# Kernel tuning notes

Measured on AMD Instinct MI355X. Metric: run time of the kernel, lower is better.

## Reference

```python
import jax, jax.numpy as jnp
import numpy as np

DEFAULT_MASK_VALUE = -0.7 * float(jnp.finfo(jnp.dtype('float32')).max)

B, T, NQ, NKV, D = 2, 1024, 32, 8, 128


def setup_inputs() -> dict:
    key = jax.random.key(0)
    k1, k2, k3, k4 = jax.random.split(key, 4)
    query = jax.random.normal(k1, (B, T, NQ, D), dtype=jnp.float32)
    kk = jax.random.normal(k2, (B, T, NKV, D), dtype=jnp.float32)
    vv = jax.random.normal(k3, (B, T, NKV, D), dtype=jnp.float32)
    # packed-sequence segment ids, sorted so each segment is contiguous (values 1..3, >0 = active)
    decoder_segment_ids = jnp.sort(jax.random.randint(k4, (B, T), 1, 4), axis=-1).astype(jnp.int32)
    return {"query": query, "key": kk, "value": vv,
            "decoder_segment_ids": decoder_segment_ids}


def _attention(query, key, value, decoder_segment_ids):
    # MaxText AttentionOp.apply_attention_dot (prefill / train mode), GQA layout.
    b, t, n, d = query.shape
    n_kv = key.shape[2]
    g = n // n_kv
    q = query.reshape(b, t, n_kv, g, d)
    # qk product: [b, n_kv, g, t, s]
    logits = jnp.einsum('btkgd,bskd->bkgts', q, key)
    # generate_attention_mask: segment mask AND causal mask
    seg_mask = decoder_segment_ids[:, :, None] == decoder_segment_ids[:, None, :]  # [b,t,s]
    row_ids = jax.lax.broadcasted_iota(jnp.int32, (t, t), 0)
    col_ids = jax.lax.broadcasted_iota(jnp.int32, (t, t), 1)
    causal = col_ids <= row_ids  # [t,s]
    mask = jnp.logical_and(seg_mask, causal[None])  # [b,t,s]
    # apply_mask_to_logits: replace masked entries with DEFAULT_MASK_VALUE (avoids add fusion)
    masked = jnp.where(mask[:, None, None, :, :], logits, DEFAULT_MASK_VALUE)
    probs = jax.nn.softmax(masked, axis=-1)
    out = jnp.einsum('bkgts,bskd->btkgd', probs, value)
    return out.reshape(b, t, n, d)


def reference(query, key, value, decoder_segment_ids):
    return _attention(query, key, value, decoder_segment_ids)
```

## Files before the change

### kernel.cpp

```cpp
#include <hip/hip_runtime.h>

constexpr int B_  = 2;
constexpr int T_  = 1024;
constexpr int NQ  = 32;
constexpr int NKV = 8;
constexpr int D_  = 128;

constexpr int BM = 64;
constexpr int BN = 64;
constexpr int NTILE = T_ / BM;
constexpr float MASK_NEG = -3.0e38f;

typedef _Float16 f16;
typedef f16 f16x4 __attribute__((ext_vector_type(4)));
typedef f16 f16x8 __attribute__((ext_vector_type(8)));
typedef float floatx4 __attribute__((ext_vector_type(4)));

__device__ __align__(16) f16 g_K16 [(size_t)B_ * NKV * T_ * D_];
__device__ __align__(16) f16 g_Vt16[(size_t)B_ * NKV * T_ * D_];

__device__ __forceinline__ void dma16(const f16* g, const f16* l) {
    __builtin_amdgcn_global_load_lds(
        (const __attribute__((address_space(1))) void*)g,
        (__attribute__((address_space(3))) void*)l, 16, 0, 0);
}

__global__ __launch_bounds__(256)
void prep_kernel(const float* __restrict__ K, const float* __restrict__ V) {
    __shared__ f16 lv[64][136];
    const int sblk = blockIdx.x;
    const int kv   = blockIdx.y;
    const int b    = blockIdx.z;
    const int tid  = threadIdx.x;
    const int s0   = sblk * 64;
    const size_t inbase = ((size_t)b * T_) * NKV * D_ + (size_t)kv * D_;

    f16* kout = g_K16 + ((size_t)(b * NKV + kv) * T_ + s0) * D_;
#pragma unroll
    for (int p = 0; p < 4; ++p) {
        const int u = tid + 256 * p;
        const int s = u >> 4, ch = u & 15;
        const float* src = K + inbase + (size_t)(s0 + s) * NKV * D_ + ch * 8;
        float4 f0 = *(const float4*)src;
        float4 f1 = *(const float4*)(src + 4);
        f16x8 hh;
        hh[0] = (f16)f0.x; hh[1] = (f16)f0.y; hh[2] = (f16)f0.z; hh[3] = (f16)f0.w;
        hh[4] = (f16)f1.x; hh[5] = (f16)f1.y; hh[6] = (f16)f1.z; hh[7] = (f16)f1.w;
        *(f16x8*)(kout + s * D_ + ((ch ^ (s & 7)) * 8)) = hh;
    }
#pragma unroll
    for (int p = 0; p < 8; ++p) {
        const int u = tid + 256 * p;
        const int s = u >> 5, d4 = u & 31;
        float4 f = *(const float4*)(V + inbase + (size_t)(s0 + s) * NKV * D_ + d4 * 4);
        f16x4 hh; hh[0] = (f16)f.x; hh[1] = (f16)f.y; hh[2] = (f16)f.z; hh[3] = (f16)f.w;
        *(f16x4*)&lv[s][d4 * 4] = hh;
    }
    __syncthreads();
    f16* vout = g_Vt16 + (size_t)((b * NKV + kv) * 16 + sblk) * 8192;
#pragma unroll
    for (int p = 0; p < 4; ++p) {
        const int u = tid + 256 * p;
        const int d = u >> 3, cu = u & 7;
        f16x8 hh;
#pragma unroll
        for (int j = 0; j < 8; ++j) hh[j] = lv[cu * 8 + j][d];
        *(f16x8*)(vout + d * 64 + ((cu ^ (d & 7)) * 8)) = hh;
    }
}

#define FA_BODY(RK, RV, WK, WV, blkv)                                          \
    {                                                                          \
        const int s0 = (blkv) * BN;                                            \
        __syncthreads();                                                       \
        if ((blkv) + 1 < nblk) {                                               \
            const f16* kt = kbase + (size_t)((blkv) + 1) * 8192 + glane;       \
            const f16* vt = vbase + (size_t)((blkv) + 1) * 8192 + glane;       \
            _Pragma("unroll")                                                  \
            for (int i = 0; i < 4; ++i) {                                      \
                dma16(kt + i * 512, WK + wbase + i * 512);                     \
                dma16(vt + i * 512, WV + wbase + i * 512);                     \
            }                                                                  \
        }                                                                      \
        floatx4 sc[4];                                                         \
        _Pragma("unroll")                                                      \
        for (int nt = 0; nt < 4; ++nt) {                                       \
            floatx4 acc = floatx4{0.f, 0.f, 0.f, 0.f};                         \
            _Pragma("unroll")                                                  \
            for (int c = 0; c < 4; ++c) {                                      \
                f16x8 kf = *(const f16x8*)(RK + (nt * 16 + ln) * 128 + kpc[c]);\
                acc = __builtin_amdgcn_mfma_f32_16x16x32_f16(qfrag[c], kf, acc, 0, 0, 0); \
            }                                                                  \
            sc[nt] = acc;                                                      \
        }                                                                      \
        _Pragma("unroll")                                                      \
        for (int nt = 0; nt < 4; ++nt) {                                       \
            const int s = s0 + nt * 16 + ln;                                   \
            const int sgs = lds_seg[s];                                        \
            _Pragma("unroll")                                                  \
            for (int r = 0; r < 4; ++r) {                                      \
                const bool ok = (s <= trow[r]) && (sgs == segq[r]);            \
                sc[nt][r] = ok ? sc[nt][r] : MASK_NEG;                         \
            }                                                                  \
        }                                                                      \
        floatx4 av;                                                            \
        _Pragma("unroll")                                                      \
        for (int r = 0; r < 4; ++r) {                                          \
            float mx = fmaxf(fmaxf(sc[0][r], sc[1][r]), fmaxf(sc[2][r], sc[3][r])); \
            mx = fmaxf(mx, __shfl_xor(mx, 1));                                 \
            mx = fmaxf(mx, __shfl_xor(mx, 2));                                 \
            mx = fmaxf(mx, __shfl_xor(mx, 4));                                 \
            mx = fmaxf(mx, __shfl_xor(mx, 8));                                 \
            const float mnew = fmaxf(m_i[r], mx);                              \
            av[r] = __expf(m_i[r] - mnew);                                     \
            m_i[r] = mnew;                                                     \
            sc[0][r] = __expf(sc[0][r] - mnew);                                \
            sc[1][r] = __expf(sc[1][r] - mnew);                                \
            sc[2][r] = __expf(sc[2][r] - mnew);                                \
            sc[3][r] = __expf(sc[3][r] - mnew);                                \
        }                                                                      \
        _Pragma("unroll")                                                      \
        for (int dt = 0; dt < 9; ++dt) o_acc[dt] *= av;                        \
        _Pragma("unroll")                                                      \
        for (int nt = 0; nt < 4; ++nt)                                         \
            _Pragma("unroll")                                                  \
            for (int r = 0; r < 4; ++r)                                        \
                lds_p[wave][quad * 4 + r][nt * 16 + ln] = (f16)sc[nt][r];      \
        __builtin_amdgcn_s_waitcnt(0xc07f);               \
        f16x8 af0 = *(const f16x8*)&lds_p[wave][ln][quad * 8];                 \
        f16x8 af1 = *(const f16x8*)&lds_p[wave][ln][32 + quad * 8];            \
        _Pragma("unroll")                                                      \
        for (int dt = 0; dt < 8; ++dt) {                                       \
            const f16* vr = RV + (dt * 16 + ln) * 64;                          \
            f16x8 b0 = *(const f16x8*)(vr + pc0);                              \
            f16x8 b1 = *(const f16x8*)(vr + pc1);                              \
            o_acc[dt] = __builtin_amdgcn_mfma_f32_16x16x32_f16(af0, b0, o_acc[dt], 0, 0, 0); \
            o_acc[dt] = __builtin_amdgcn_mfma_f32_16x16x32_f16(af1, b1, o_acc[dt], 0, 0, 0); \
        }                                                                      \
        o_acc[8] = __builtin_amdgcn_mfma_f32_16x16x32_f16(af0, vones, o_acc[8], 0, 0, 0); \
        o_acc[8] = __builtin_amdgcn_mfma_f32_16x16x32_f16(af1, vones, o_acc[8], 0, 0, 0); \
    }

__global__ __launch_bounds__(256, 2)
void fa_kernel(const float* __restrict__ Qg, const int* __restrict__ seg,
               float* __restrict__ Og) {
    __shared__ __align__(16) f16 kb0[64 * 128];
    __shared__ __align__(16) f16 kb1[64 * 128];
    __shared__ __align__(16) f16 vb0[128 * 64];
    __shared__ __align__(16) f16 vb1[128 * 64];
    __shared__ f16 lds_p[4][16][72];
    __shared__ int lds_seg[T_];

    const int pair = blockIdx.x;
    const int h    = blockIdx.y;
    const int b    = blockIdx.z;
    const int kv   = h >> 2;

    const int tid  = threadIdx.x;
    const int wave = tid >> 6;
    const int lane = tid & 63;
    const int quad = lane >> 4;
    const int ln   = lane & 15;
    const int sw   = ln & 7;

    int kpc[4];
#pragma unroll
    for (int c = 0; c < 4; ++c) kpc[c] = ((4 * c + quad) ^ sw) * 8;
    const int pc0 = (quad ^ sw) * 8;
    const int pc1 = ((quad + 4) ^ sw) * 8;

    const int glane = wave * 2048 + lane * 8;
    const int wbase = wave * 2048;

    const f16* kbase = g_K16 + (size_t)(b * NKV + kv) * T_ * D_;
    const f16* vbase = g_Vt16 + (size_t)(b * NKV + kv) * T_ * D_;

    *(int4*)&lds_seg[tid * 4] = *(const int4*)(seg + b * T_ + tid * 4);

    f16x8 vones;
#pragma unroll
    for (int j = 0; j < 8; ++j) vones[j] = (f16)1.0f;

    for (int sub = 0; sub < 2; ++sub) {
        const int tile = sub ? pair : (NTILE - 1 - pair);
        const int t0 = tile * BM;

        const int qrow = t0 + wave * 16 + ln;
        const float* qptr = Qg + (((size_t)b * T_ + qrow) * NQ + h) * D_;
        f16x8 qfrag[4];
#pragma unroll
        for (int c = 0; c < 4; ++c) {
            const float* p = qptr + c * 32 + quad * 8;
            float4 f0 = *(const float4*)(p);
            float4 f1 = *(const float4*)(p + 4);
            f16x8 v;
            v[0] = (f16)f0.x; v[1] = (f16)f0.y; v[2] = (f16)f0.z; v[3] = (f16)f0.w;
            v[4] = (f16)f1.x; v[5] = (f16)f1.y; v[6] = (f16)f1.z; v[7] = (f16)f1.w;
            qfrag[c] = v;
        }

        __syncthreads();

        int trow[4], segq[4];
#pragma unroll
        for (int r = 0; r < 4; ++r) {
            trow[r] = t0 + wave * 16 + quad * 4 + r;
            segq[r] = lds_seg[trow[r]];
        }
        const int seg_lo = lds_seg[t0];

        unsigned long long bal = __ballot(lds_seg[lane * 16 + 15] < seg_lo);
        const int blk_start = __popcll(bal) >> 2;
        const int nblk = tile + 1;

        float  m_i[4];
        floatx4 o_acc[9];
#pragma unroll
        for (int r = 0; r < 4; ++r) m_i[r] = -1.0e30f;
#pragma unroll
        for (int dt = 0; dt < 9; ++dt) o_acc[dt] = floatx4{0.f, 0.f, 0.f, 0.f};

        {
            const f16* kt = kbase + (size_t)blk_start * 8192 + glane;
            const f16* vt = vbase + (size_t)blk_start * 8192 + glane;
#pragma unroll
            for (int i = 0; i < 4; ++i) {
                dma16(kt + i * 512, kb0 + wbase + i * 512);
                dma16(vt + i * 512, vb0 + wbase + i * 512);
            }
        }

        int blk = blk_start;
        while (true) {
            FA_BODY(kb0, vb0, kb1, vb1, blk)
            if (++blk >= nblk) break;
            FA_BODY(kb1, vb1, kb0, vb0, blk)
            if (++blk >= nblk) break;
        }

#pragma unroll
        for (int r = 0; r < 4; ++r) {
            const float inv = 1.0f / o_acc[8][r];
            float* optr = Og + (((size_t)b * T_ + trow[r]) * NQ + h) * D_ + ln;
#pragma unroll
            for (int dt = 0; dt < 8; ++dt)
                optr[dt * 16] = o_acc[dt][r] * inv;
        }
    }
}

extern "C" void kernel_launch(void* const* d_in, const int* in_sizes, int n_in,
                              void* d_out, int out_size, void* d_ws, size_t ws_size,
                              hipStream_t stream) {
    const float* Q   = (const float*)d_in[0];
    const float* K   = (const float*)d_in[1];
    const float* V   = (const float*)d_in[2];
    const int*   seg = (const int*)d_in[3];
    float* out = (float*)d_out;

    dim3 pgrid(NTILE, NKV, B_);
    prep_kernel<<<pgrid, 256, 0, stream>>>(K, V);

    dim3 grid(NTILE / 2, NQ, B_);
    fa_kernel<<<grid, 256, 0, stream>>>(Q, seg, out);
}
```

Measured before the change: 127.2 us.

## Compute transposed QK scores and shuffle P into MFMA fragments in registers

Swaps the MFMA operands so each lane holds scores for a single query row, which reduces the row max to two cross-lane shuffles and gives one running max per lane. The P matrix is packed to fp16 pairs and rearranged across lanes with xor shuffles instead of a round trip through an LDS staging buffer. The per-column segment compare is replaced by a range check against each row's segment start, found by binary search over the segment ids, which relies on segments being contiguous. The rescale factors are moved back to the output layout with ds_bpermute, which adds shuffle traffic in place of LDS stores and loads.

Result: faster. 124.6 us (-2.0%).

```diff
diff --git a/kernel.cpp b/kernel.cpp
--- a/kernel.cpp
+++ b/kernel.cpp
@@ -12,9 +12,11 @@
 constexpr float MASK_NEG = -3.0e38f;
 
 typedef _Float16 f16;
+typedef __fp16 fp16_2 __attribute__((ext_vector_type(2)));
 typedef f16 f16x4 __attribute__((ext_vector_type(4)));
 typedef f16 f16x8 __attribute__((ext_vector_type(8)));
 typedef float floatx4 __attribute__((ext_vector_type(4)));
+typedef unsigned int uintx4 __attribute__((ext_vector_type(4)));
 
 __device__ __align__(16) f16 g_K16 [(size_t)B_ * NKV * T_ * D_];
 __device__ __align__(16) f16 g_Vt16[(size_t)B_ * NKV * T_ * D_];
@@ -23,6 +25,30 @@
     __builtin_amdgcn_global_load_lds(
         (const __attribute__((address_space(1))) void*)g,
         (__attribute__((address_space(3))) void*)l, 16, 0, 0);
+}
+
+__device__ __forceinline__ void swap32(unsigned &a, unsigned &b) {
+    unsigned ax = (unsigned)__shfl_xor((int)a, 32);
+    unsigned bx = (unsigned)__shfl_xor((int)b, 32);
+    const bool hi = (threadIdx.x & 32) != 0;
+    unsigned na = hi ? bx : a;
+    unsigned nb = hi ? b  : ax;
+    a = na; b = nb;
+}
+
+__device__ __forceinline__ void swap16(unsigned &a, unsigned &b) {
+    unsigned ax = (unsigned)__shfl_xor((int)a, 16);
+    unsigned bx = (unsigned)__shfl_xor((int)b, 16);
+    const bool odd = (threadIdx.x & 16) != 0;
+    unsigned na = odd ? bx : a;
+    unsigned nb = odd ? b  : ax;
+    a = na; b = nb;
+}
+
+__device__ __forceinline__ unsigned pk2(float a, float b) {
+    union { fp16_2 h; unsigned u; } c;
+    c.h = __builtin_amdgcn_cvt_pkrtz(a, b);
+    return c.u;
 }
 
 __global__ __launch_bounds__(256)
@@ -89,46 +115,58 @@
             _Pragma("unroll")                                                  \
             for (int c = 0; c < 4; ++c) {                                      \
                 f16x8 kf = *(const f16x8*)(RK + (nt * 16 + ln) * 128 + kpc[c]);\
-                acc = __builtin_amdgcn_mfma_f32_16x16x32_f16(qfrag[c], kf, acc, 0, 0, 0); \
+                acc = __builtin_amdgcn_mfma_f32_16x16x32_f16(kf, qfrag[c], acc, 0, 0, 0); \
             }                                                                  \
             sc[nt] = acc;                                                      \
         }                                                                      \
         _Pragma("unroll")                                                      \
         for (int nt = 0; nt < 4; ++nt) {                                       \
-            const int s = s0 + nt * 16 + ln;                                   \
-            const int sgs = lds_seg[s];                                        \
             _Pragma("unroll")                                                  \
             for (int r = 0; r < 4; ++r) {                                      \
-                const bool ok = (s <= trow[r]) && (sgs == segq[r]);            \
+                const int s = s0 + nt * 16 + quad * 4 + r;                     \
+                const bool ok = (s <= qrow_l) && (s >= fs_l);                  \
                 sc[nt][r] = ok ? sc[nt][r] : MASK_NEG;                         \
             }                                                                  \
         }                                                                      \
-        floatx4 av;                                                            \
-        _Pragma("unroll")                                                      \
-        for (int r = 0; r < 4; ++r) {                                          \
-            float mx = fmaxf(fmaxf(sc[0][r], sc[1][r]), fmaxf(sc[2][r], sc[3][r])); \
-            mx = fmaxf(mx, __shfl_xor(mx, 1));                                 \
-            mx = fmaxf(mx, __shfl_xor(mx, 2));                                 \
-            mx = fmaxf(mx, __shfl_xor(mx, 4));                                 \
-            mx = fmaxf(mx, __shfl_xor(mx, 8));                                 \
-            const float mnew = fmaxf(m_i[r], mx);                              \
-            av[r] = __expf(m_i[r] - mnew);                                     \
-            m_i[r] = mnew;                                                     \
-            sc[0][r] = __expf(sc[0][r] - mnew);                                \
-            sc[1][r] = __expf(sc[1][r] - mnew);                                \
-            sc[2][r] = __expf(sc[2][r] - mnew);                                \
-            sc[3][r] = __expf(sc[3][r] - mnew);                                \
-        }                                                                      \
-        _Pragma("unroll")                                                      \
-        for (int dt = 0; dt < 9; ++dt) o_acc[dt] *= av;                        \
-        _Pragma("unroll")                                                      \
-        for (int nt = 0; nt < 4; ++nt)                                         \
-            _Pragma("unroll")                                                  \
-            for (int r = 0; r < 4; ++r)                                        \
-                lds_p[wave][quad * 4 + r][nt * 16 + ln] = (f16)sc[nt][r];      \
-        __builtin_amdgcn_s_waitcnt(0xc07f);               \
-        f16x8 af0 = *(const f16x8*)&lds_p[wave][ln][quad * 8];                 \
-        f16x8 af1 = *(const f16x8*)&lds_p[wave][ln][32 + quad * 8];            \
+        float mx = fmaxf(                                                      \
+            fmaxf(fmaxf(fmaxf(sc[0][0], sc[0][1]), fmaxf(sc[0][2], sc[0][3])), \
+                  fmaxf(fmaxf(sc[1][0], sc[1][1]), fmaxf(sc[1][2], sc[1][3]))),\
+            fmaxf(fmaxf(fmaxf(sc[2][0], sc[2][1]), fmaxf(sc[2][2], sc[2][3])), \
+                  fmaxf(fmaxf(sc[3][0], sc[3][1]), fmaxf(sc[3][2], sc[3][3]))));\
+        mx = fmaxf(mx, __shfl_xor(mx, 16));                                    \
+        mx = fmaxf(mx, __shfl_xor(mx, 32));                                    \
+        const float mnew = fmaxf(m_i, mx);                                     \
+        const float av = __expf(m_i - mnew);                                   \
+        m_i = mnew;                                                            \
+        _Pragma("unroll")                                                      \
+        for (int nt = 0; nt < 4; ++nt) {                                       \
+            sc[nt][0] = __expf(sc[nt][0] - mnew);                              \
+            sc[nt][1] = __expf(sc[nt][1] - mnew);                              \
+            sc[nt][2] = __expf(sc[nt][2] - mnew);                              \
+            sc[nt][3] = __expf(sc[nt][3] - mnew);                              \
+        }                                                                      \
+        const int avi = __float_as_int(av);                                    \
+        floatx4 avr;                                                           \
+        _Pragma("unroll")                                                      \
+        for (int r = 0; r < 4; ++r)                                            \
+            avr[r] = __int_as_float(__builtin_amdgcn_ds_bpermute(bpbase + 4 * r, avi)); \
+        _Pragma("unroll")                                                      \
+        for (int dt = 0; dt < 9; ++dt) o_acc[dt] *= avr;                       \
+        unsigned Da[4], Db[4];                                                 \
+        _Pragma("unroll")                                                      \
+        for (int nt = 0; nt < 4; ++nt) {                                       \
+            Da[nt] = pk2(sc[nt][0], sc[nt][1]);                                \
+            Db[nt] = pk2(sc[nt][2], sc[nt][3]);                                \
+        }                                                                      \
+        swap32(Da[0], Da[1]); swap32(Db[0], Db[1]);                            \
+        swap16(Da[0], Da[1]); swap16(Db[0], Db[1]);                            \
+        swap32(Da[2], Da[3]); swap32(Db[2], Db[3]);                            \
+        swap16(Da[2], Da[3]); swap16(Db[2], Db[3]);                            \
+        union { uintx4 u; f16x8 h; } c0_, c1_;                                 \
+        c0_.u = uintx4{Da[0], Db[0], Da[1], Db[1]};                            \
+        c1_.u = uintx4{Da[2], Db[2], Da[3], Db[3]};                            \
+        const f16x8 af0 = c0_.h;                                               \
+        const f16x8 af1 = c1_.h;                                               \
         _Pragma("unroll")                                                      \
         for (int dt = 0; dt < 8; ++dt) {                                       \
             const f16* vr = RV + (dt * 16 + ln) * 64;                          \
@@ -148,7 +186,6 @@
     __shared__ __align__(16) f16 kb1[64 * 128];
     __shared__ __align__(16) f16 vb0[128 * 64];
     __shared__ __align__(16) f16 vb1[128 * 64];
-    __shared__ f16 lds_p[4][16][72];
     __shared__ int lds_seg[T_];
 
     const int pair = blockIdx.x;
@@ -168,6 +205,7 @@
     for (int c = 0; c < 4; ++c) kpc[c] = ((4 * c + quad) ^ sw) * 8;
     const int pc0 = (quad ^ sw) * 8;
     const int pc1 = ((quad + 4) ^ sw) * 8;
+    const int bpbase = quad << 4;
 
     const int glane = wave * 2048 + lane * 8;
     const int wbase = wave * 2048;
@@ -201,22 +239,26 @@
 
         __syncthreads();
 
-        int trow[4], segq[4];
-#pragma unroll
-        for (int r = 0; r < 4; ++r) {
-            trow[r] = t0 + wave * 16 + quad * 4 + r;
-            segq[r] = lds_seg[trow[r]];
-        }
+        int trow[4];
+#pragma unroll
+        for (int r = 0; r < 4; ++r) trow[r] = t0 + wave * 16 + quad * 4 + r;
+
+        const int qrow_l = qrow;
+        const int segq_l = lds_seg[qrow_l];
+        int lo = 0, hi = qrow_l;
+        while (lo < hi) {
+            const int mid = (lo + hi) >> 1;
+            if (lds_seg[mid] < segq_l) lo = mid + 1; else hi = mid;
+        }
+        const int fs_l = lo;
+
         const int seg_lo = lds_seg[t0];
-
         unsigned long long bal = __ballot(lds_seg[lane * 16 + 15] < seg_lo);
         const int blk_start = __popcll(bal) >> 2;
         const int nblk = tile + 1;
 
-        float  m_i[4];
+        float  m_i = -1.0e30f;
         floatx4 o_acc[9];
-#pragma unroll
-        for (int r = 0; r < 4; ++r) m_i[r] = -1.0e30f;
 #pragma unroll
         for (int dt = 0; dt < 9; ++dt) o_acc[dt] = floatx4{0.f, 0.f, 0.f, 0.f};
 
```

## Use 128-row Q tiles with transposed S^T MFMA keeping P in registers

Applied to the files above, without the earlier changes.

Doubles the query tile to 128 rows, with each wave handling two 16-row groups that share the K/V fragments loaded from LDS. QK^T is computed transposed (K as the A operand) so the softmax probabilities land in the register layout the PV MFMA (16x16x16) expects. This removes the LDS round-trip for P and the ones-column MFMA used to get the row sum, which is now tracked as a scalar l_i. The segment mask becomes a per-row first-segment-start bound found by binary search, and blocks are ordered with a diagonal tile assignment instead of pairing heavy and light tiles. The cost is more registers per wave and possible load imbalance across tiles of different causal length.

After: 121.1 us. 4.8% less time.

```diff
diff --git a/kernel.cpp b/kernel.cpp
--- a/kernel.cpp
+++ b/kernel.cpp
@@ -6,12 +6,13 @@
 constexpr int NKV = 8;
 constexpr int D_  = 128;
 
-constexpr int BM = 64;
+constexpr int BM = 128;
 constexpr int BN = 64;
 constexpr int NTILE = T_ / BM;
 constexpr float MASK_NEG = -3.0e38f;
 
 typedef _Float16 f16;
+typedef __fp16 fp16_2 __attribute__((ext_vector_type(2)));
 typedef f16 f16x4 __attribute__((ext_vector_type(4)));
 typedef f16 f16x8 __attribute__((ext_vector_type(8)));
 typedef float floatx4 __attribute__((ext_vector_type(4)));
@@ -23,6 +24,12 @@
     __builtin_amdgcn_global_load_lds(
         (const __attribute__((address_space(1))) void*)g,
         (__attribute__((address_space(3))) void*)l, 16, 0, 0);
+}
+
+__device__ __forceinline__ unsigned pk2(float a, float b) {
+    union { fp16_2 h; unsigned u; } c;
+    c.h = __builtin_amdgcn_cvt_pkrtz(a, b);
+    return c.u;
 }
 
 __global__ __launch_bounds__(256)
@@ -82,63 +89,76 @@
                 dma16(vt + i * 512, WV + wbase + i * 512);                     \
             }                                                                  \
         }                                                                      \
-        floatx4 sc[4];                                                         \
+        floatx4 sc[2][4];                                                      \
         _Pragma("unroll")                                                      \
         for (int nt = 0; nt < 4; ++nt) {                                       \
-            floatx4 acc = floatx4{0.f, 0.f, 0.f, 0.f};                         \
-            _Pragma("unroll")                                                  \
-            for (int c = 0; c < 4; ++c) {                                      \
-                f16x8 kf = *(const f16x8*)(RK + (nt * 16 + ln) * 128 + kpc[c]);\
-                acc = __builtin_amdgcn_mfma_f32_16x16x32_f16(qfrag[c], kf, acc, 0, 0, 0); \
-            }                                                                  \
-            sc[nt] = acc;                                                      \
-        }                                                                      \
+            f16x8 kf[4];                                                       \
+            _Pragma("unroll")                                                  \
+            for (int c = 0; c < 4; ++c)                                        \
+                kf[c] = *(const f16x8*)(RK + (nt * 16 + ln) * 128 + kpc[c]);   \
+            _Pragma("unroll")                                                  \
+            for (int qn = 0; qn < 2; ++qn) {                                   \
+                floatx4 acc = floatx4{0.f, 0.f, 0.f, 0.f};                     \
+                _Pragma("unroll")                                              \
+                for (int c = 0; c < 4; ++c)                                    \
+                    acc = __builtin_amdgcn_mfma_f32_16x16x32_f16(kf[c], qfrag[qn][c], acc, 0, 0, 0); \
+                sc[qn][nt] = acc;                                              \
+            }                                                                  \
+        }                                                                      \
+        f16x4 pf[2][4];                                                        \
         _Pragma("unroll")                                                      \
-        for (int nt = 0; nt < 4; ++nt) {                                       \
-            const int s = s0 + nt * 16 + ln;                                   \
-            const int sgs = lds_seg[s];                                        \
-            _Pragma("unroll")                                                  \
-            for (int r = 0; r < 4; ++r) {                                      \
-                const bool ok = (s <= trow[r]) && (sgs == segq[r]);            \
-                sc[nt][r] = ok ? sc[nt][r] : MASK_NEG;                         \
-            }                                                                  \
-        }                                                                      \
-        floatx4 av;                                                            \
-        _Pragma("unroll")                                                      \
-        for (int r = 0; r < 4; ++r) {                                          \
-            float mx = fmaxf(fmaxf(sc[0][r], sc[1][r]), fmaxf(sc[2][r], sc[3][r])); \
-            mx = fmaxf(mx, __shfl_xor(mx, 1));                                 \
-            mx = fmaxf(mx, __shfl_xor(mx, 2));                                 \
-            mx = fmaxf(mx, __shfl_xor(mx, 4));                                 \
-            mx = fmaxf(mx, __shfl_xor(mx, 8));                                 \
-            const float mnew = fmaxf(m_i[r], mx);                              \
-            av[r] = __expf(m_i[r] - mnew);                                     \
-            m_i[r] = mnew;                                                     \
-            sc[0][r] = __expf(sc[0][r] - mnew);                                \
-            sc[1][r] = __expf(sc[1][r] - mnew);                                \
-            sc[2][r] = __expf(sc[2][r] - mnew);                                \
-            sc[3][r] = __expf(sc[3][r] - mnew);                                \
-        }                                                                      \
-        _Pragma("unroll")                                                      \
-        for (int dt = 0; dt < 9; ++dt) o_acc[dt] *= av;                        \
-        _Pragma("unroll")                                                      \
-        for (int nt = 0; nt < 4; ++nt)                                         \
-            _Pragma("unroll")                                                  \
-            for (int r = 0; r < 4; ++r)                                        \
-                lds_p[wave][quad * 4 + r][nt * 16 + ln] = (f16)sc[nt][r];      \
-        __builtin_amdgcn_s_waitcnt(0xc07f);               \
-        f16x8 af0 = *(const f16x8*)&lds_p[wave][ln][quad * 8];                 \
-        f16x8 af1 = *(const f16x8*)&lds_p[wave][ln][32 + quad * 8];            \
+        for (int qn = 0; qn < 2; ++qn) {                                       \
+            _Pragma("unroll")                                                  \
+            for (int nt = 0; nt < 4; ++nt) {                                   \
+                _Pragma("unroll")                                              \
+                for (int r = 0; r < 4; ++r) {                                  \
+                    const int s = s0 + nt * 16 + quad * 4 + r;                 \
+                    const bool ok = (s <= qrow_l[qn]) && (s >= fs_l[qn]);      \
+                    sc[qn][nt][r] = ok ? sc[qn][nt][r] : MASK_NEG;             \
+                }                                                              \
+            }                                                                  \
+            float mx = fmaxf(                                                  \
+                fmaxf(fmaxf(fmaxf(sc[qn][0][0], sc[qn][0][1]), fmaxf(sc[qn][0][2], sc[qn][0][3])), \
+                      fmaxf(fmaxf(sc[qn][1][0], sc[qn][1][1]), fmaxf(sc[qn][1][2], sc[qn][1][3]))), \
+                fmaxf(fmaxf(fmaxf(sc[qn][2][0], sc[qn][2][1]), fmaxf(sc[qn][2][2], sc[qn][2][3])), \
+                      fmaxf(fmaxf(sc[qn][3][0], sc[qn][3][1]), fmaxf(sc[qn][3][2], sc[qn][3][3])))); \
+            mx = fmaxf(mx, __shfl_xor(mx, 16));                                \
+            mx = fmaxf(mx, __shfl_xor(mx, 32));                                \
+            const float mnew = fmaxf(m_i[qn], mx);                             \
+            const float av = __expf(m_i[qn] - mnew);                           \
+            m_i[qn] = mnew;                                                    \
+            float ts = 0.f;                                                    \
+            _Pragma("unroll")                                                  \
+            for (int nt = 0; nt < 4; ++nt) {                                   \
+                _Pragma("unroll")                                              \
+                for (int r = 0; r < 4; ++r) {                                  \
+                    sc[qn][nt][r] = __expf(sc[qn][nt][r] - mnew);              \
+                    ts += sc[qn][nt][r];                                       \
+                }                                                              \
+            }                                                                  \
+            ts += __shfl_xor(ts, 16);                                          \
+            ts += __shfl_xor(ts, 32);                                          \
+            l_i[qn] = l_i[qn] * av + ts;                                       \
+            _Pragma("unroll")                                                  \
+            for (int dt = 0; dt < 8; ++dt) o_acc[qn][dt] *= av;                \
+            _Pragma("unroll")                                                  \
+            for (int nt = 0; nt < 4; ++nt) {                                   \
+                union { unsigned u[2]; f16x4 h; } pu;                          \
+                pu.u[0] = pk2(sc[qn][nt][0], sc[qn][nt][1]);                   \
+                pu.u[1] = pk2(sc[qn][nt][2], sc[qn][nt][3]);                   \
+                pf[qn][nt] = pu.h;                                             \
+            }                                                                  \
+        }                                                                      \
         _Pragma("unroll")                                                      \
         for (int dt = 0; dt < 8; ++dt) {                                       \
             const f16* vr = RV + (dt * 16 + ln) * 64;                          \
-            f16x8 b0 = *(const f16x8*)(vr + pc0);                              \
-            f16x8 b1 = *(const f16x8*)(vr + pc1);                              \
-            o_acc[dt] = __builtin_amdgcn_mfma_f32_16x16x32_f16(af0, b0, o_acc[dt], 0, 0, 0); \
-            o_acc[dt] = __builtin_amdgcn_mfma_f32_16x16x32_f16(af1, b1, o_acc[dt], 0, 0, 0); \
-        }                                                                      \
-        o_acc[8] = __builtin_amdgcn_mfma_f32_16x16x32_f16(af0, vones, o_acc[8], 0, 0, 0); \
-        o_acc[8] = __builtin_amdgcn_mfma_f32_16x16x32_f16(af1, vones, o_acc[8], 0, 0, 0); \
+            _Pragma("unroll")                                                  \
+            for (int nt = 0; nt < 4; ++nt) {                                   \
+                f16x4 va = *(const f16x4*)(vr + vpc[nt]);                      \
+                o_acc[0][dt] = __builtin_amdgcn_mfma_f32_16x16x16f16(va, pf[0][nt], o_acc[0][dt], 0, 0, 0); \
+                o_acc[1][dt] = __builtin_amdgcn_mfma_f32_16x16x16f16(va, pf[1][nt], o_acc[1][dt], 0, 0, 0); \
+            }                                                                  \
+        }                                                                      \
     }
 
 __global__ __launch_bounds__(256, 2)
@@ -148,10 +168,10 @@
     __shared__ __align__(16) f16 kb1[64 * 128];
     __shared__ __align__(16) f16 vb0[128 * 64];
     __shared__ __align__(16) f16 vb1[128 * 64];
-    __shared__ f16 lds_p[4][16][72];
     __shared__ int lds_seg[T_];
 
-    const int pair = blockIdx.x;
+    const int xt   = (int)((blockIdx.x + blockIdx.y) & 7);
+    const int tile = blockIdx.z ? (7 - xt) : xt;
     const int h    = blockIdx.y;
     const int b    = blockIdx.z;
     const int kv   = h >> 2;
@@ -166,8 +186,10 @@
     int kpc[4];
 #pragma unroll
     for (int c = 0; c < 4; ++c) kpc[c] = ((4 * c + quad) ^ sw) * 8;
-    const int pc0 = (quad ^ sw) * 8;
-    const int pc1 = ((quad + 4) ^ sw) * 8;
+    int vpc[4];
+#pragma unroll
+    for (int nt = 0; nt < 4; ++nt)
+        vpc[nt] = (((2 * nt + (quad >> 1)) ^ sw) * 8) + (quad & 1) * 4;
 
     const int glane = wave * 2048 + lane * 8;
     const int wbase = wave * 2048;
@@ -177,17 +199,14 @@
 
     *(int4*)&lds_seg[tid * 4] = *(const int4*)(seg + b * T_ + tid * 4);
 
-    f16x8 vones;
-#pragma unroll
-    for (int j = 0; j < 8; ++j) vones[j] = (f16)1.0f;
-
-    for (int sub = 0; sub < 2; ++sub) {
-        const int tile = sub ? pair : (NTILE - 1 - pair);
-        const int t0 = tile * BM;
-
-        const int qrow = t0 + wave * 16 + ln;
-        const float* qptr = Qg + (((size_t)b * T_ + qrow) * NQ + h) * D_;
-        f16x8 qfrag[4];
+    const int t0 = tile * BM;
+
+    int qrow_l[2];
+    f16x8 qfrag[2][4];
+#pragma unroll
+    for (int qn = 0; qn < 2; ++qn) {
+        qrow_l[qn] = t0 + wave * 32 + qn * 16 + ln;
+        const float* qptr = Qg + (((size_t)b * T_ + qrow_l[qn]) * NQ + h) * D_;
 #pragma unroll
         for (int c = 0; c < 4; ++c) {
             const float* p = qptr + c * 32 + quad * 8;
@@ -196,55 +215,64 @@
             f16x8 v;
             v[0] = (f16)f0.x; v[1] = (f16)f0.y; v[2] = (f16)f0.z; v[3] = (f16)f0.w;
             v[4] = (f16)f1.x; v[5] = (f16)f1.y; v[6] = (f16)f1.z; v[7] = (f16)f1.w;
-            qfrag[c] = v;
-        }
-
-        __syncthreads();
-
-        int trow[4], segq[4];
-#pragma unroll
-        for (int r = 0; r < 4; ++r) {
-            trow[r] = t0 + wave * 16 + quad * 4 + r;
-            segq[r] = lds_seg[trow[r]];
-        }
-        const int seg_lo = lds_seg[t0];
-
-        unsigned long long bal = __ballot(lds_seg[lane * 16 + 15] < seg_lo);
-        const int blk_start = __popcll(bal) >> 2;
-        const int nblk = tile + 1;
-
-        float  m_i[4];
-        floatx4 o_acc[9];
-#pragma unroll
-        for (int r = 0; r < 4; ++r) m_i[r] = -1.0e30f;
-#pragma unroll
-        for (int dt = 0; dt < 9; ++dt) o_acc[dt] = floatx4{0.f, 0.f, 0.f, 0.f};
-
-        {
-            const f16* kt = kbase + (size_t)blk_start * 8192 + glane;
-            const f16* vt = vbase + (size_t)blk_start * 8192 + glane;
-#pragma unroll
-            for (int i = 0; i < 4; ++i) {
-                dma16(kt + i * 512, kb0 + wbase + i * 512);
-                dma16(vt + i * 512, vb0 + wbase + i * 512);
-            }
-        }
-
-        int blk = blk_start;
-        while (true) {
-            FA_BODY(kb0, vb0, kb1, vb1, blk)
-            if (++blk >= nblk) break;
-            FA_BODY(kb1, vb1, kb0, vb0, blk)
-            if (++blk >= nblk) break;
-        }
-
-#pragma unroll
-        for (int r = 0; r < 4; ++r) {
-            const float inv = 1.0f / o_acc[8][r];
-            float* optr = Og + (((size_t)b * T_ + trow[r]) * NQ + h) * D_ + ln;
-#pragma unroll
-            for (int dt = 0; dt < 8; ++dt)
-                optr[dt * 16] = o_acc[dt][r] * inv;
+            qfrag[qn][c] = v;
+        }
+    }
+
+    __syncthreads();
+
+    int fs_l[2];
+#pragma unroll
+    for (int qn = 0; qn < 2; ++qn) {
+        const int segq = lds_seg[qrow_l[qn]];
+        int lo = 0, hi = qrow_l[qn];
+        while (lo < hi) {
+            const int mid = (lo + hi) >> 1;
+            if (lds_seg[mid] < segq) lo = mid + 1; else hi = mid;
+        }
+        fs_l[qn] = lo;
+    }
+
+    const int seg_lo = lds_seg[t0];
+    unsigned long long bal = __ballot(lds_seg[lane * 16 + 15] < seg_lo);
+    const int blk_start = __popcll(bal) >> 2;
+    const int nblk = 2 * (tile + 1);
+
+    float  m_i[2] = { -1.0e30f, -1.0e30f };
+    float  l_i[2] = { 0.f, 0.f };
+    floatx4 o_acc[2][8];
+#pragma unroll
+    for (int qn = 0; qn < 2; ++qn)
+#pragma unroll
+        for (int dt = 0; dt < 8; ++dt) o_acc[qn][dt] = floatx4{0.f, 0.f, 0.f, 0.f};
+
+    {
+        const f16* kt = kbase + (size_t)blk_start * 8192 + glane;
+        const f16* vt = vbase + (size_t)blk_start * 8192 + glane;
+#pragma unroll
+        for (int i = 0; i < 4; ++i) {
+            dma16(kt + i * 512, kb0 + wbase + i * 512);
+            dma16(vt + i * 512, vb0 + wbase + i * 512);
+        }
+    }
+
+    int blk = blk_start;
+    while (true) {
+        FA_BODY(kb0, vb0, kb1, vb1, blk)
+        if (++blk >= nblk) break;
+        FA_BODY(kb1, vb1, kb0, vb0, blk)
+        if (++blk >= nblk) break;
+    }
+
+#pragma unroll
+    for (int qn = 0; qn < 2; ++qn) {
+        const float inv = 1.0f / l_i[qn];
+        float* optr = Og + (((size_t)b * T_ + qrow_l[qn]) * NQ + h) * D_;
+#pragma unroll
+        for (int dt = 0; dt < 8; ++dt) {
+            floatx4 o = o_acc[qn][dt];
+            o[0] *= inv; o[1] *= inv; o[2] *= inv; o[3] *= inv;
+            *(floatx4*)(optr + dt * 16 + quad * 4) = o;
         }
     }
 }
@@ -258,9 +286,9 @@
     const int*   seg = (const int*)d_in[3];
     float* out = (float*)d_out;
 
-    dim3 pgrid(NTILE, NKV, B_);
+    dim3 pgrid(16, NKV, B_);
     prep_kernel<<<pgrid, 256, 0, stream>>>(K, V);
 
-    dim3 grid(NTILE / 2, NQ, B_);
+    dim3 grid(NTILE, NQ, B_);
     fa_kernel<<<grid, 256, 0, stream>>>(Q, seg, out);
 }
```
